# Kernel tuning notes

Hardware: AMD Instinct MI355X
Metric: run time of the kernel (lower is better)

The kernel has to match this reference:

```python
import jax, jax.numpy as jnp
import numpy as np

EPS = 1e-13


def _masked_softmax(logits, mask_last):
    # logits: [B, Q, K]; mask_last: [B, 1, K] float {0,1}
    # Faithful to torch source: multiply logits by mask (NOT additive -inf),
    # softmax, re-mask, renormalize.
    p = jax.nn.softmax(logits * mask_last, axis=-1) * mask_last
    return p / (jnp.sum(p, axis=-1, keepdims=True) + EPS)


def setup_inputs() -> dict:
    key = jax.random.key(0)
    k1, k2, k3, k4 = jax.random.split(key, 4)
    B, LA, LB, H = 16, 1024, 1024, 512
    premise_batch = jax.random.normal(k1, (B, LA, H), dtype=jnp.float32)
    hypothesis_batch = jax.random.normal(k2, (B, LB, H), dtype=jnp.float32)
    premise_mask = jax.random.randint(k3, (B, LA), 0, 2).astype(jnp.float32)
    hypothesis_mask = jax.random.randint(k4, (B, LB), 0, 2).astype(jnp.float32)
    # avoid fully-masked rows (degenerate)
    premise_mask = premise_mask.at[:, 0].set(1.0)
    hypothesis_mask = hypothesis_mask.at[:, 0].set(1.0)
    return {
        "premise_batch": premise_batch,
        "premise_mask": premise_mask,
        "hypothesis_batch": hypothesis_batch,
        "hypothesis_mask": hypothesis_mask,
    }


def reference(premise_batch, premise_mask, hypothesis_batch, hypothesis_mask):
    # sim[b,i,j] = <a_i, b_j>
    sim = jnp.einsum("bih,bjh->bij", premise_batch, hypothesis_batch)
    prem_hyp_attn = _masked_softmax(sim, hypothesis_mask[:, None, :])           # [B,LA,LB]
    hyp_prem_attn = _masked_softmax(sim.transpose(0, 2, 1), premise_mask[:, None, :])  # [B,LB,LA]
    attended_premises = jnp.einsum("bij,bjh->bih", prem_hyp_attn, hypothesis_batch)
    attended_premises = attended_premises * premise_mask[:, :, None]
    attended_hypotheses = jnp.einsum("bji,bjh->bih", hyp_prem_attn.transpose(0, 2, 1), premise_batch)
    attended_hypotheses = attended_hypotheses * hypothesis_mask[:, :, None]
    return (attended_premises, attended_hypotheses)
```

## Files before the change

### kernel.cpp

```cpp
#include <hip/hip_runtime.h>
#include <hip/hip_fp16.h>
#include <math.h>

#define NB   16
#define SLA  1024
#define SLB  1024
#define HH   512

typedef __attribute__((ext_vector_type(4))) float  f32x4;
typedef __attribute__((ext_vector_type(8))) short  s16x8;
typedef __attribute__((ext_vector_type(4))) int    i32x4;

#define QS    (6.5f / 127.f)
#define QINVS (127.f / 6.5f)

__device__ __forceinline__ unsigned short f2bf(float x){
  unsigned u = __float_as_uint(x);
  u += 0x7fffu + ((u >> 16) & 1u);
  return (unsigned short)(u >> 16);
}
__device__ __forceinline__ float bf2f(unsigned short h){
  return __uint_as_float(((unsigned)h) << 16);
}
__device__ __forceinline__ float h2f(unsigned short h){
  return __half2float(__ushort_as_half(h));
}
__device__ __forceinline__ unsigned fkey(float f){
  unsigned u = __float_as_uint(f);
  return ((int)u < 0) ? ~u : (u | 0x80000000u);
}
__device__ __forceinline__ float funkey(unsigned k){
  return __uint_as_float((k & 0x80000000u) ? (k & 0x7fffffffu) : ~k);
}

__device__ __forceinline__ void gl2lds16(const void* g, void* l){
  __builtin_amdgcn_global_load_lds(
      (__attribute__((address_space(1))) unsigned int*)(unsigned long long)(size_t)g,
      (__attribute__((address_space(3))) unsigned int*)(unsigned int)(size_t)l,
      16, 0, 0);
}

__global__ __launch_bounds__(256) void scan_kernel(
    const float* __restrict__ pmask, const float* __restrict__ hmask,
    int* __restrict__ pIdx, int* __restrict__ hIdx,
    int* __restrict__ pCnt, int* __restrict__ hCnt,
    int* __restrict__ pPad, int* __restrict__ hPad,
    unsigned* __restrict__ rowMaxU, unsigned* __restrict__ colMaxU,
    float* __restrict__ colSum)
{
  __shared__ int ps[256];
  const int b     = blockIdx.x;
  const int which = blockIdx.y;
  const int t     = threadIdx.x;
  const float* m = (which ? hmask : pmask) + b * 1024;
  int* idx = (which ? hIdx : pIdx) + b * 1024;
  int* cnt = which ? hCnt : pCnt;
  int* pad = which ? hPad : pPad;

  #pragma unroll
  for (int v = 0; v < 4; ++v){
    int g = b * 1024 + t + v * 256;
    if (which == 0){
      rowMaxU[g] = 0u;
    } else {
      colMaxU[g] = 0u;
      colSum[g]  = 0.f;
    }
  }

  int f[4], s = 0;
  #pragma unroll
  for (int e = 0; e < 4; ++e){
    f[e] = m[t * 4 + e] > 0.5f ? 1 : 0;
    s += f[e];
  }
  ps[t] = s;
  __syncthreads();
  for (int off = 1; off < 256; off <<= 1){
    int v = (t >= off) ? ps[t - off] : 0;
    __syncthreads();
    ps[t] += v;
    __syncthreads();
  }
  int pos = ps[t] - s;
  #pragma unroll
  for (int e = 0; e < 4; ++e){
    if (f[e]) idx[pos++] = t * 4 + e;
  }
  if (t == 0){
    int total = ps[255];
    cnt[b] = total;
    pad[b] = (total + 127) & ~127;
  }
}

__global__ __launch_bounds__(256) void zero_out_kernel(
    const float* __restrict__ pmask, const float* __restrict__ hmask,
    float* __restrict__ out)
{
  const int r = blockIdx.x * 4 + (threadIdx.x >> 6);
  const int side = r >> 14;
  const int b    = (r >> 10) & 15;
  const int row  = r & 1023;
  const float mv = (side ? hmask : pmask)[b * 1024 + row];
  if (mv > 0.5f) return;
  float4 z = {0.f, 0.f, 0.f, 0.f};
  float* p = out + (size_t)side * NB * SLA * HH
                 + ((size_t)b * 1024 + row) * 512 + (threadIdx.x & 63) * 8;
  *(float4*)p = z;
  *(float4*)(p + 4) = z;
}

__global__ __launch_bounds__(256) void cvt_gather_kernel(
    const float* __restrict__ prem, const float* __restrict__ hyp,
    const int* __restrict__ pIdx, const int* __restrict__ hIdx,
    const int* __restrict__ pCnt, const int* __restrict__ hCnt,
    const int* __restrict__ pPad, const int* __restrict__ hPad,
    char* __restrict__ premD1, char* __restrict__ premD0,
    char* __restrict__ hypD1,  char* __restrict__ hypD0,
    unsigned short* __restrict__ PremT, unsigned short* __restrict__ HypT)
{
  __shared__ unsigned short tv[64][72];
  __shared__ int sIdx[64];

  const int tensor = blockIdx.z >> 4;
  const int b  = blockIdx.z & 15;
  const int l0 = blockIdx.y * 64;
  const int h0 = blockIdx.x * 64;
  const int t  = threadIdx.x;

  const int cnt = tensor ? hCnt[b] : pCnt[b];
  const int pad = tensor ? hPad[b] : pPad[b];
  if (l0 >= pad) return;

  const float* X = tensor ? hyp : prem;
  const int* idx = (tensor ? hIdx : pIdx) + b * 1024;
  char* D1 = tensor ? hypD1 : premD1;
  char* D0 = tensor ? hypD0 : premD0;
  unsigned short* XT = tensor ? HypT : PremT;

  if (t < 64){
    int jc = l0 + t;
    sIdx[t] = (jc < cnt) ? idx[jc] : -1;
  }
  __syncthreads();

  #pragma unroll
  for (int it = 0; it < 4; ++it){
    int r = (t >> 4) + it * 16;
    int c = (t & 15) * 4;
    int orig = sIdx[r];
    float4 x = {0.f, 0.f, 0.f, 0.f};
    if (orig >= 0)
      x = *(const float4*)(X + ((size_t)b * 1024 + orig) * HH + h0 + c);
    float xv[4] = {x.x, x.y, x.z, x.w};
    char d1v[4], d0v[4];
    #pragma unroll
    for (int e = 0; e < 4; ++e){
      float xs = xv[e] * QINVS;
      float x1 = rintf(xs);
      x1 = fminf(127.f, fmaxf(-127.f, x1));
      float x0 = rintf((xs - x1) * 256.f);
      x0 = fminf(127.f, fmaxf(-128.f, x0));
      d1v[e] = (char)(int)x1;
      d0v[e] = (char)(int)x0;
      tv[c + e][r] = f2bf(xv[e]);
    }
    size_t go = ((size_t)b * 1024 + l0 + r) * HH + h0 + c;
    *(char4*)(D1 + go) = make_char4(d1v[0], d1v[1], d1v[2], d1v[3]);
    *(char4*)(D0 + go) = make_char4(d0v[0], d0v[1], d0v[2], d0v[3]);
  }
  __syncthreads();
  const int w   = t >> 2;
  const int seg = (t & 3) * 16;
  const uint4* src = (const uint4*)&tv[w][seg];
  uint4* dst = (uint4*)(XT + ((size_t)b * HH + h0 + w) * 1024 + l0 + seg);
  dst[0] = src[0];
  dst[1] = src[1];
}

__global__ __launch_bounds__(256, 3) void sim_gemm_v5_kernel(
    const char* __restrict__ premD1, const char* __restrict__ premD0,
    const char* __restrict__ hypD1,  const char* __restrict__ hypD0,
    const int* __restrict__ pCnt, const int* __restrict__ hCnt,
    const int* __restrict__ pPad, const int* __restrict__ hPad,
    unsigned short* __restrict__ simH,
    unsigned* __restrict__ rowMaxU, unsigned* __restrict__ colMaxU)
{
  __shared__ char sA1[128 * 64];
  __shared__ char sA0[128 * 64];
  __shared__ char sB1[64 * 64];
  __shared__ char sB0[64 * 64];

  const int b  = blockIdx.z;
  const int i0 = blockIdx.y * 128;
  const int j0 = blockIdx.x * 64;
  const int t  = threadIdx.x;

  const int pc = pCnt[b], hc = hCnt[b];
  if (i0 >= pPad[b] || j0 >= hPad[b]) return;

  const char* A1 = premD1 + ((size_t)b * 1024 + i0) * HH;
  const char* A0 = premD0 + ((size_t)b * 1024 + i0) * HH;
  const char* B1 = hypD1  + ((size_t)b * 1024 + j0) * HH;
  const char* B0 = hypD0  + ((size_t)b * 1024 + j0) * HH;

  const int sr = t >> 2;
  const int gc = ((t & 3) ^ (sr & 3)) * 16;
  const int lco = (t & 3) * 16;

  const int lane = t & 63;
  const int wr = (t >> 7) & 1;
  const int wc = (t >> 6) & 1;
  const int q  = lane >> 4;
  const int ln = lane & 15;
  const int fo = (q ^ (ln & 3)) * 16;

  i32x4 acc1[4][2], accc[4][2];
  #pragma unroll
  for (int mt = 0; mt < 4; ++mt)
    #pragma unroll
    for (int nt = 0; nt < 2; ++nt){
      acc1[mt][nt] = (i32x4){0, 0, 0, 0};
      accc[mt][nt] = (i32x4){0, 0, 0, 0};
    }

  for (int k0 = 0; k0 < HH; k0 += 64){
    __syncthreads();
    {
      const size_t goA = (size_t)sr * HH + k0 + gc;
      gl2lds16(A1 + goA, &sA1[sr * 64 + lco]);
      gl2lds16(A0 + goA, &sA0[sr * 64 + lco]);
      const size_t goA2 = (size_t)(64 + sr) * HH + k0 + gc;
      gl2lds16(A1 + goA2, &sA1[(64 + sr) * 64 + lco]);
      gl2lds16(A0 + goA2, &sA0[(64 + sr) * 64 + lco]);
      gl2lds16(B1 + goA, &sB1[sr * 64 + lco]);
      gl2lds16(B0 + goA, &sB0[sr * 64 + lco]);
    }
    __syncthreads();

    i32x4 af[4], bf1[2], bf0[2];
    #pragma unroll
    for (int mt = 0; mt < 4; ++mt)
      af[mt] = *(const i32x4*)&sA1[(wr * 64 + mt * 16 + ln) * 64 + fo];
    #pragma unroll
    for (int nt = 0; nt < 2; ++nt)
      bf1[nt] = *(const i32x4*)&sB1[(wc * 32 + nt * 16 + ln) * 64 + fo];
    #pragma unroll
    for (int mt = 0; mt < 4; ++mt)
      #pragma unroll
      for (int nt = 0; nt < 2; ++nt)
        acc1[mt][nt] = __builtin_amdgcn_mfma_i32_16x16x64_i8(af[mt], bf1[nt], acc1[mt][nt], 0, 0, 0);
    #pragma unroll
    for (int nt = 0; nt < 2; ++nt)
      bf0[nt] = *(const i32x4*)&sB0[(wc * 32 + nt * 16 + ln) * 64 + fo];
    #pragma unroll
    for (int mt = 0; mt < 4; ++mt)
      #pragma unroll
      for (int nt = 0; nt < 2; ++nt)
        accc[mt][nt] = __builtin_amdgcn_mfma_i32_16x16x64_i8(af[mt], bf0[nt], accc[mt][nt], 0, 0, 0);
    #pragma unroll
    for (int mt = 0; mt < 4; ++mt)
      af[mt] = *(const i32x4*)&sA0[(wr * 64 + mt * 16 + ln) * 64 + fo];
    #pragma unroll
    for (int mt = 0; mt < 4; ++mt)
      #pragma unroll
      for (int nt = 0; nt < 2; ++nt)
        accc[mt][nt] = __builtin_amdgcn_mfma_i32_16x16x64_i8(af[mt], bf1[nt], accc[mt][nt], 0, 0, 0);
  }

  const float S2 = QS * QS;
  unsigned short* simb = simH + ((size_t)b * SLA + i0) * SLB + j0;

  float rmx[16];
  #pragma unroll
  for (int e = 0; e < 16; ++e) rmx[e] = -1e30f;
  float cmx[2];
  cmx[0] = -1e30f; cmx[1] = -1e30f;

  #pragma unroll
  for (int mt = 0; mt < 4; ++mt){
    #pragma unroll
    for (int nt = 0; nt < 2; ++nt){
      int col = wc * 32 + nt * 16 + ln;
      bool colv = (j0 + col) < hc;
      #pragma unroll
      for (int rr = 0; rr < 4; ++rr){
        int row = wr * 64 + mt * 16 + q * 4 + rr;
        float f = S2 * ((float)acc1[mt][nt][rr] + (float)accc[mt][nt][rr] * 0.00390625f);
        simb[(size_t)row * SLB + col] = __half_as_ushort(__float2half(f));
        rmx[mt * 4 + rr] = fmaxf(rmx[mt * 4 + rr], colv ? f : -1e30f);
        cmx[nt] = fmaxf(cmx[nt], (i0 + row) < pc ? f : -1e30f);
      }
    }
  }

  #pragma unroll
  for (int e = 0; e < 16; ++e){
    float v = rmx[e];
    v = fmaxf(v, __shfl_xor(v, 1));
    v = fmaxf(v, __shfl_xor(v, 2));
    v = fmaxf(v, __shfl_xor(v, 4));
    v = fmaxf(v, __shfl_xor(v, 8));
    if (ln == 0){
      int row = wr * 64 + (e >> 2) * 16 + q * 4 + (e & 3);
      if (i0 + row < pc)
        atomicMax(rowMaxU + b * 1024 + i0 + row, fkey(v));
    }
  }
  #pragma unroll
  for (int nt = 0; nt < 2; ++nt){
    float v = cmx[nt];
    v = fmaxf(v, __shfl_xor(v, 16));
    v = fmaxf(v, __shfl_xor(v, 32));
    if (q == 0){
      int col = wc * 32 + nt * 16 + ln;
      if (j0 + col < hc)
        atomicMax(colMaxU + b * 1024 + j0 + col, fkey(v));
    }
  }
}

__global__ __launch_bounds__(256) void build_pt_kernel(
    const unsigned short* __restrict__ simH,
    const unsigned* __restrict__ colMaxU,
    const int* __restrict__ pCnt, const int* __restrict__ hCnt,
    const int* __restrict__ pPad, const int* __restrict__ hPad,
    unsigned short* __restrict__ PhypT, float* __restrict__ colSum)
{
  __shared__ unsigned short tp[64][72];
  __shared__ float sCM[64];

  const int b  = blockIdx.z;
  const int i0 = blockIdx.y * 64;
  const int j0 = blockIdx.x * 64;
  const int t  = threadIdx.x;

  const int pc = pCnt[b], hc = hCnt[b];
  if (i0 >= pPad[b] || j0 >= hPad[b]) return;

  if (t < 64) sCM[t] = funkey(colMaxU[b * 1024 + j0 + t]);
  __syncthreads();

  const unsigned short* sb = simH + (size_t)b * SLA * SLB;
  #pragma unroll
  for (int it = 0; it < 4; ++it){
    int r = (t >> 4) + it * 16;
    int c = (t & 15) * 4;
    uint2 u = *(const uint2*)(sb + (size_t)(i0 + r) * SLB + j0 + c);
    float s0 = h2f((unsigned short)(u.x & 0xffff));
    float s1 = h2f((unsigned short)(u.x >> 16));
    float s2 = h2f((unsigned short)(u.y & 0xffff));
    float s3 = h2f((unsigned short)(u.y >> 16));
    bool vi = (i0 + r) < pc;
    tp[c + 0][r] = f2bf((vi && (j0 + c + 0) < hc) ? __expf(s0 - sCM[c+0]) : 0.f);
    tp[c + 1][r] = f2bf((vi && (j0 + c + 1) < hc) ? __expf(s1 - sCM[c+1]) : 0.f);
    tp[c + 2][r] = f2bf((vi && (j0 + c + 2) < hc) ? __expf(s2 - sCM[c+2]) : 0.f);
    tp[c + 3][r] = f2bf((vi && (j0 + c + 3) < hc) ? __expf(s3 - sCM[c+3]) : 0.f);
  }
  __syncthreads();
  const int w   = t >> 2;
  const int seg = (t & 3) * 16;
  const uint4* src = (const uint4*)&tp[w][seg];
  uint4 u0 = src[0], u1 = src[1];
  uint4* dst = (uint4*)(PhypT + ((size_t)b * 1024 + j0 + w) * 1024 + i0 + seg);
  dst[0] = u0;
  dst[1] = u1;

  const unsigned short* us0 = (const unsigned short*)&u0;
  const unsigned short* us1 = (const unsigned short*)&u1;
  float cs = 0.f;
  #pragma unroll
  for (int e = 0; e < 8; ++e) cs += bf2f(us0[e]);
  #pragma unroll
  for (int e = 0; e < 8; ++e) cs += bf2f(us1[e]);
  cs += __shfl_xor(cs, 1);
  cs += __shfl_xor(cs, 2);
  if ((t & 3) == 0 && (j0 + w) < hc)
    atomicAdd(colSum + b * 1024 + j0 + w, cs);
}

__global__ __launch_bounds__(256, 4) void av2_kernel(
    const unsigned short* __restrict__ simH,
    const unsigned short* __restrict__ PhypT,
    const unsigned short* __restrict__ HypT, const unsigned short* __restrict__ PremT,
    const unsigned* __restrict__ rowMaxU, const float* __restrict__ colSum,
    const int* __restrict__ pIdx, const int* __restrict__ hIdx,
    const int* __restrict__ pCnt, const int* __restrict__ hCnt,
    const int* __restrict__ pPad, const int* __restrict__ hPad,
    float* __restrict__ out)
{
  __shared__ unsigned short sA[128 * 64];
  __shared__ unsigned short sB[128 * 64];
  __shared__ float sRM[128];
  __shared__ float sScale[128];
  __shared__ int   sIdx[128];

  const int side = blockIdx.z >> 4;
  const int b    = blockIdx.z & 15;
  const int m0   = blockIdx.y * 128;
  const int n0   = blockIdx.x * 128;
  const int t    = threadIdx.x;

  const int cnt  = side ? hCnt[b] : pCnt[b];
  const int hc   = hCnt[b];
  const int mpad = side ? hPad[b] : pPad[b];
  const int kpad = side ? pPad[b] : hPad[b];
  if (m0 >= mpad) return;

  const int* idx = (side ? hIdx : pIdx) + b * 1024;
  float* o = out + (size_t)side * NB * SLA * HH + (size_t)b * 1024 * 512;

  if (t < 128){
    sIdx[t] = idx[m0 + t];
    if (side){
      sScale[t] = 1.f / colSum[b * 1024 + m0 + t];
    } else {
      sRM[t] = funkey(rowMaxU[b * 1024 + m0 + t]);
    }
  }

  const int wv = t >> 6;
  const int L  = t & 63;
  const int lr = L >> 3;
  const int sw = L & 7;
  const int gkc = (sw ^ lr) * 8;

  const int ar  = t >> 1;
  const int akh = (t & 1) * 32;

  const int lane = t & 63;
  const int wr = (t >> 7) & 1;
  const int wc = (t >> 6) & 1;
  const int q  = lane >> 4;
  const int ln = lane & 15;
  const int fsw = ln & 7;

  const unsigned short* simb  = simH  + (size_t)b * 1024 * 1024;
  const unsigned short* Ahyp  = PhypT + (size_t)b * 1024 * 1024;
  const unsigned short* Bt    = (side ? PremT : HypT) + (size_t)b * 512 * 1024;

  float rs = 0.f;

  f32x4 acc[4][4];
  #pragma unroll
  for (int mt = 0; mt < 4; ++mt)
    #pragma unroll
    for (int nt = 0; nt < 4; ++nt)
      acc[mt][nt] = (f32x4){0.f, 0.f, 0.f, 0.f};

  for (int k0 = 0; k0 < kpad; k0 += 64){
    __syncthreads();
    if (side == 0){
      #pragma unroll
      for (int s = 0; s < 4; ++s){
        int row = wv * 32 + s * 8 + lr;
        gl2lds16(Bt + (size_t)(n0 + row) * 1024 + k0 + gkc, &sB[row * 64 + sw * 8]);
      }
      const unsigned short* sp = simb + (size_t)(m0 + ar) * 1024 + k0 + akh;
      float rm = sRM[ar];
      #pragma unroll
      for (int cc = 0; cc < 4; ++cc){
        uint4 u = *(const uint4*)(sp + cc * 8);
        unsigned uw[4] = {u.x, u.y, u.z, u.w};
        int kb = k0 + akh + cc * 8;
        unsigned short pb[8];
        #pragma unroll
        for (int d = 0; d < 4; ++d){
          float v0 = h2f((unsigned short)(uw[d] & 0xffff));
          float v1 = h2f((unsigned short)(uw[d] >> 16));
          float p0 = (kb + d * 2 + 0) < hc ? __expf(v0 - rm) : 0.f;
          float p1 = (kb + d * 2 + 1) < hc ? __expf(v1 - rm) : 0.f;
          rs += p0 + p1;
          pb[d * 2]     = f2bf(p0);
          pb[d * 2 + 1] = f2bf(p1);
        }
        uint4 w;
        w.x = (unsigned)pb[0] | ((unsigned)pb[1] << 16);
        w.y = (unsigned)pb[2] | ((unsigned)pb[3] << 16);
        w.z = (unsigned)pb[4] | ((unsigned)pb[5] << 16);
        w.w = (unsigned)pb[6] | ((unsigned)pb[7] << 16);
        int c   = (t & 1) * 4 + cc;
        int pos = c ^ (ar & 7);
        *(uint4*)&sA[ar * 64 + pos * 8] = w;
      }
    } else {
      #pragma unroll
      for (int s = 0; s < 4; ++s){
        int row = wv * 32 + s * 8 + lr;
        gl2lds16(Ahyp + (size_t)(m0 + row) * 1024 + k0 + gkc, &sA[row * 64 + sw * 8]);
        gl2lds16(Bt   + (size_t)(n0 + row) * 1024 + k0 + gkc, &sB[row * 64 + sw * 8]);
      }
    }
    __syncthreads();

    #pragma unroll
    for (int h = 0; h < 2; ++h){
      s16x8 af[4], bfr[4];
      #pragma unroll
      for (int mt = 0; mt < 4; ++mt){
        int r = wr * 64 + mt * 16 + ln;
        af[mt] = *(const s16x8*)&sA[r * 64 + (((h << 2) + q) ^ fsw) * 8];
      }
      #pragma unroll
      for (int nt = 0; nt < 4; ++nt){
        int r = wc * 64 + nt * 16 + ln;
        bfr[nt] = *(const s16x8*)&sB[r * 64 + (((h << 2) + q) ^ fsw) * 8];
      }
      #pragma unroll
      for (int mt = 0; mt < 4; ++mt)
        #pragma unroll
        for (int nt = 0; nt < 4; ++nt)
          acc[mt][nt] = __builtin_amdgcn_mfma_f32_16x16x32_bf16(af[mt], bfr[nt], acc[mt][nt], 0, 0, 0);
    }
  }

  if (side == 0){
    rs += __shfl_xor(rs, 1);
    __syncthreads();
    if ((t & 1) == 0) sScale[ar] = 1.f / rs;
    __syncthreads();
  }

  #pragma unroll
  for (int mt = 0; mt < 4; ++mt)
    #pragma unroll
    for (int nt = 0; nt < 4; ++nt){
      int col = n0 + wc * 64 + nt * 16 + ln;
      #pragma unroll
      for (int rr = 0; rr < 4; ++rr){
        int rowL = wr * 64 + mt * 16 + q * 4 + rr;
        if (m0 + rowL < cnt)
          o[(size_t)sIdx[rowL] * 512 + col] = acc[mt][nt][rr] * sScale[rowL];
      }
    }
}

extern "C" void kernel_launch(void* const* d_in, const int* in_sizes, int n_in,
                              void* d_out, int out_size, void* d_ws, size_t ws_size,
                              hipStream_t stream)
{
  const float* prem  = (const float*)d_in[0];
  const float* pmask = (const float*)d_in[1];
  const float* hyp   = (const float*)d_in[2];
  const float* hmask = (const float*)d_in[3];
  float* out = (float*)d_out;

  char* ws = (char*)d_ws;
  unsigned short* simH = (unsigned short*)(ws);
  unsigned* rowMaxU = (unsigned*)(ws + 67108864);
  unsigned* colMaxU = (unsigned*)(ws + 67108864 + 2 * 65536);
  float*    colSum  = (float*)(ws + 67108864 + 3 * 65536);
  int* pIdx = (int*)(ws + 67108864 + 4 * 65536);
  int* hIdx = (int*)(ws + 67108864 + 5 * 65536);
  int* pCnt = (int*)(ws + 67108864 + 6 * 65536);
  int* hCnt = (int*)(ws + 67108864 + 6 * 65536 + 256);
  int* pPad = (int*)(ws + 67108864 + 6 * 65536 + 512);
  int* hPad = (int*)(ws + 67108864 + 6 * 65536 + 768);
  const size_t base2 = 67108864 + 4 * 65536 + 1048576;
  char* premD1 = (char*)(ws + base2);
  char* premD0 = (char*)(ws + base2 + 8388608);
  char* hypD1  = (char*)(ws + base2 + 16777216);
  char* hypD0  = (char*)(ws + base2 + 25165824);
  unsigned short* PremT = (unsigned short*)(ws + base2 + 33554432);
  unsigned short* HypT  = (unsigned short*)(ws + base2 + 50331648);
  unsigned short* PhypT = (unsigned short*)(ws + base2);
  const size_t need = base2 + 100663296;
  if (ws_size < need) return;

  scan_kernel<<<dim3(16, 2), 256, 0, stream>>>(pmask, hmask, pIdx, hIdx,
                                               pCnt, hCnt, pPad, hPad,
                                               rowMaxU, colMaxU, colSum);
  zero_out_kernel<<<dim3(8192), 256, 0, stream>>>(pmask, hmask, out);
  cvt_gather_kernel<<<dim3(8, 16, 32), 256, 0, stream>>>(
      prem, hyp, pIdx, hIdx, pCnt, hCnt, pPad, hPad,
      premD1, premD0, hypD1, hypD0, PremT, HypT);
  sim_gemm_v5_kernel<<<dim3(16, 8, NB), 256, 0, stream>>>(
      premD1, premD0, hypD1, hypD0, pCnt, hCnt, pPad, hPad,
      simH, rowMaxU, colMaxU);
  build_pt_kernel<<<dim3(16, 16, NB), 256, 0, stream>>>(
      simH, colMaxU, pCnt, hCnt, pPad, hPad, PhypT, colSum);
  av2_kernel<<<dim3(4, 8, 32), 256, 0, stream>>>(
      simH, PhypT, HypT, PremT, rowMaxU, colSum,
      pIdx, hIdx, pCnt, hCnt, pPad, hPad, out);
}
```

Baseline: 210.1 us.

## Write transposed sim in GEMM epilogue and drop separate build_pt pass

The sim GEMM epilogue now also writes a transposed fp16 copy of the similarity tile through an LDS staging buffer that reuses the operand shared memory. The later attention-value kernel treats both sides the same way, computing exp and row sums on the fly from either simH or simT. This removes the build_pt kernel and its colSum atomics, trading that extra full pass over the sim matrix for additional stores in the GEMM and exp work on the hypothesis side of the AV kernel.

```diff
diff --git a/kernel.cpp b/kernel.cpp
--- a/kernel.cpp
+++ b/kernel.cpp
@@ -45,8 +45,7 @@
     int* __restrict__ pIdx, int* __restrict__ hIdx,
     int* __restrict__ pCnt, int* __restrict__ hCnt,
     int* __restrict__ pPad, int* __restrict__ hPad,
-    unsigned* __restrict__ rowMaxU, unsigned* __restrict__ colMaxU,
-    float* __restrict__ colSum)
+    unsigned* __restrict__ rowMaxU, unsigned* __restrict__ colMaxU)
 {
   __shared__ int ps[256];
   const int b     = blockIdx.x;
@@ -64,7 +63,6 @@
       rowMaxU[g] = 0u;
     } else {
       colMaxU[g] = 0u;
-      colSum[g]  = 0.f;
     }
   }
 
@@ -179,18 +177,28 @@
   dst[1] = src[1];
 }
 
-__global__ __launch_bounds__(256, 3) void sim_gemm_v5_kernel(
+__global__ __launch_bounds__(256, 3) void sim_gemm_v6_kernel(
     const char* __restrict__ premD1, const char* __restrict__ premD0,
     const char* __restrict__ hypD1,  const char* __restrict__ hypD0,
     const int* __restrict__ pCnt, const int* __restrict__ hCnt,
     const int* __restrict__ pPad, const int* __restrict__ hPad,
-    unsigned short* __restrict__ simH,
+    unsigned short* __restrict__ simH, unsigned short* __restrict__ simT,
     unsigned* __restrict__ rowMaxU, unsigned* __restrict__ colMaxU)
 {
-  __shared__ char sA1[128 * 64];
-  __shared__ char sA0[128 * 64];
-  __shared__ char sB1[64 * 64];
-  __shared__ char sB0[64 * 64];
+  union __align__(16) Smem {
+    struct {
+      char A1[128 * 64];
+      char A0[128 * 64];
+      char B1[64 * 64];
+      char B0[64 * 64];
+    } g;
+    unsigned short tp[64][136];
+  };
+  __shared__ Smem su;
+#define sA1 (su.g.A1)
+#define sA0 (su.g.A0)
+#define sB1 (su.g.B1)
+#define sB0 (su.g.B0)
 
   const int b  = blockIdx.z;
   const int i0 = blockIdx.y * 128;
@@ -278,21 +286,41 @@
   float cmx[2];
   cmx[0] = -1e30f; cmx[1] = -1e30f;
 
+  __syncthreads();
+
   #pragma unroll
   for (int mt = 0; mt < 4; ++mt){
     #pragma unroll
     for (int nt = 0; nt < 2; ++nt){
       int col = wc * 32 + nt * 16 + ln;
       bool colv = (j0 + col) < hc;
+      unsigned short hv[4];
       #pragma unroll
       for (int rr = 0; rr < 4; ++rr){
         int row = wr * 64 + mt * 16 + q * 4 + rr;
         float f = S2 * ((float)acc1[mt][nt][rr] + (float)accc[mt][nt][rr] * 0.00390625f);
-        simb[(size_t)row * SLB + col] = __half_as_ushort(__float2half(f));
+        unsigned short hb = __half_as_ushort(__float2half(f));
+        simb[(size_t)row * SLB + col] = hb;
+        hv[rr] = hb;
         rmx[mt * 4 + rr] = fmaxf(rmx[mt * 4 + rr], colv ? f : -1e30f);
         cmx[nt] = fmaxf(cmx[nt], (i0 + row) < pc ? f : -1e30f);
       }
-    }
+      uint2 w;
+      w.x = (unsigned)hv[0] | ((unsigned)hv[1] << 16);
+      w.y = (unsigned)hv[2] | ((unsigned)hv[3] << 16);
+      *(uint2*)&su.tp[col][wr * 64 + mt * 16 + q * 4] = w;
+    }
+  }
+  __syncthreads();
+  {
+    const int jr  = t >> 2;
+    const int seg = (t & 3) * 32;
+    const uint4* src = (const uint4*)&su.tp[jr][seg];
+    uint4* dst = (uint4*)(simT + ((size_t)b * SLB + j0 + jr) * SLA + i0 + seg);
+    dst[0] = src[0];
+    dst[1] = src[1];
+    dst[2] = src[2];
+    dst[3] = src[3];
   }
 
   #pragma unroll
@@ -319,72 +347,17 @@
         atomicMax(colMaxU + b * 1024 + j0 + col, fkey(v));
     }
   }
-}
-
-__global__ __launch_bounds__(256) void build_pt_kernel(
+#undef sA1
+#undef sA0
+#undef sB1
+#undef sB0
+}
+
+__global__ __launch_bounds__(256, 4) void av3_kernel(
     const unsigned short* __restrict__ simH,
-    const unsigned* __restrict__ colMaxU,
-    const int* __restrict__ pCnt, const int* __restrict__ hCnt,
-    const int* __restrict__ pPad, const int* __restrict__ hPad,
-    unsigned short* __restrict__ PhypT, float* __restrict__ colSum)
-{
-  __shared__ unsigned short tp[64][72];
-  __shared__ float sCM[64];
-
-  const int b  = blockIdx.z;
-  const int i0 = blockIdx.y * 64;
-  const int j0 = blockIdx.x * 64;
-  const int t  = threadIdx.x;
-
-  const int pc = pCnt[b], hc = hCnt[b];
-  if (i0 >= pPad[b] || j0 >= hPad[b]) return;
-
-  if (t < 64) sCM[t] = funkey(colMaxU[b * 1024 + j0 + t]);
-  __syncthreads();
-
-  const unsigned short* sb = simH + (size_t)b * SLA * SLB;
-  #pragma unroll
-  for (int it = 0; it < 4; ++it){
-    int r = (t >> 4) + it * 16;
-    int c = (t & 15) * 4;
-    uint2 u = *(const uint2*)(sb + (size_t)(i0 + r) * SLB + j0 + c);
-    float s0 = h2f((unsigned short)(u.x & 0xffff));
-    float s1 = h2f((unsigned short)(u.x >> 16));
-    float s2 = h2f((unsigned short)(u.y & 0xffff));
-    float s3 = h2f((unsigned short)(u.y >> 16));
-    bool vi = (i0 + r) < pc;
-    tp[c + 0][r] = f2bf((vi && (j0 + c + 0) < hc) ? __expf(s0 - sCM[c+0]) : 0.f);
-    tp[c + 1][r] = f2bf((vi && (j0 + c + 1) < hc) ? __expf(s1 - sCM[c+1]) : 0.f);
-    tp[c + 2][r] = f2bf((vi && (j0 + c + 2) < hc) ? __expf(s2 - sCM[c+2]) : 0.f);
-    tp[c + 3][r] = f2bf((vi && (j0 + c + 3) < hc) ? __expf(s3 - sCM[c+3]) : 0.f);
-  }
-  __syncthreads();
-  const int w   = t >> 2;
-  const int seg = (t & 3) * 16;
-  const uint4* src = (const uint4*)&tp[w][seg];
-  uint4 u0 = src[0], u1 = src[1];
-  uint4* dst = (uint4*)(PhypT + ((size_t)b * 1024 + j0 + w) * 1024 + i0 + seg);
-  dst[0] = u0;
-  dst[1] = u1;
-
-  const unsigned short* us0 = (const unsigned short*)&u0;
-  const unsigned short* us1 = (const unsigned short*)&u1;
-  float cs = 0.f;
-  #pragma unroll
-  for (int e = 0; e < 8; ++e) cs += bf2f(us0[e]);
-  #pragma unroll
-  for (int e = 0; e < 8; ++e) cs += bf2f(us1[e]);
-  cs += __shfl_xor(cs, 1);
-  cs += __shfl_xor(cs, 2);
-  if ((t & 3) == 0 && (j0 + w) < hc)
-    atomicAdd(colSum + b * 1024 + j0 + w, cs);
-}
-
-__global__ __launch_bounds__(256, 4) void av2_kernel(
-    const unsigned short* __restrict__ simH,
-    const unsigned short* __restrict__ PhypT,
+    const unsigned short* __restrict__ simT,
     const unsigned short* __restrict__ HypT, const unsigned short* __restrict__ PremT,
-    const unsigned* __restrict__ rowMaxU, const float* __restrict__ colSum,
+    const unsigned* __restrict__ rowMaxU, const unsigned* __restrict__ colMaxU,
     const int* __restrict__ pIdx, const int* __restrict__ hIdx,
     const int* __restrict__ pCnt, const int* __restrict__ hCnt,
     const int* __restrict__ pPad, const int* __restrict__ hPad,
@@ -403,9 +376,9 @@
   const int t    = threadIdx.x;
 
   const int cnt  = side ? hCnt[b] : pCnt[b];
-  const int hc   = hCnt[b];
   const int mpad = side ? hPad[b] : pPad[b];
   const int kpad = side ? pPad[b] : hPad[b];
+  const int kcnt = side ? pCnt[b] : hCnt[b];
   if (m0 >= mpad) return;
 
   const int* idx = (side ? hIdx : pIdx) + b * 1024;
@@ -413,11 +386,7 @@
 
   if (t < 128){
     sIdx[t] = idx[m0 + t];
-    if (side){
-      sScale[t] = 1.f / colSum[b * 1024 + m0 + t];
-    } else {
-      sRM[t] = funkey(rowMaxU[b * 1024 + m0 + t]);
-    }
+    sRM[t]  = funkey((side ? colMaxU : rowMaxU)[b * 1024 + m0 + t]);
   }
 
   const int wv = t >> 6;
@@ -436,9 +405,8 @@
   const int ln = lane & 15;
   const int fsw = ln & 7;
 
-  const unsigned short* simb  = simH  + (size_t)b * 1024 * 1024;
-  const unsigned short* Ahyp  = PhypT + (size_t)b * 1024 * 1024;
-  const unsigned short* Bt    = (side ? PremT : HypT) + (size_t)b * 512 * 1024;
+  const unsigned short* As = (side ? simT : simH) + (size_t)b * 1024 * 1024;
+  const unsigned short* Bt = (side ? PremT : HypT) + (size_t)b * 512 * 1024;
 
   float rs = 0.f;
 
@@ -451,13 +419,13 @@
 
   for (int k0 = 0; k0 < kpad; k0 += 64){
     __syncthreads();
-    if (side == 0){
-      #pragma unroll
-      for (int s = 0; s < 4; ++s){
-        int row = wv * 32 + s * 8 + lr;
-        gl2lds16(Bt + (size_t)(n0 + row) * 1024 + k0 + gkc, &sB[row * 64 + sw * 8]);
-      }
-      const unsigned short* sp = simb + (size_t)(m0 + ar) * 1024 + k0 + akh;
+    #pragma unroll
+    for (int s = 0; s < 4; ++s){
+      int row = wv * 32 + s * 8 + lr;
+      gl2lds16(Bt + (size_t)(n0 + row) * 1024 + k0 + gkc, &sB[row * 64 + sw * 8]);
+    }
+    {
+      const unsigned short* sp = As + (size_t)(m0 + ar) * 1024 + k0 + akh;
       float rm = sRM[ar];
       #pragma unroll
       for (int cc = 0; cc < 4; ++cc){
@@ -469,8 +437,8 @@
         for (int d = 0; d < 4; ++d){
           float v0 = h2f((unsigned short)(uw[d] & 0xffff));
           float v1 = h2f((unsigned short)(uw[d] >> 16));
-          float p0 = (kb + d * 2 + 0) < hc ? __expf(v0 - rm) : 0.f;
-          float p1 = (kb + d * 2 + 1) < hc ? __expf(v1 - rm) : 0.f;
+          float p0 = (kb + d * 2 + 0) < kcnt ? __expf(v0 - rm) : 0.f;
+          float p1 = (kb + d * 2 + 1) < kcnt ? __expf(v1 - rm) : 0.f;
           rs += p0 + p1;
           pb[d * 2]     = f2bf(p0);
           pb[d * 2 + 1] = f2bf(p1);
@@ -484,13 +452,6 @@
         int pos = c ^ (ar & 7);
         *(uint4*)&sA[ar * 64 + pos * 8] = w;
       }
-    } else {
-      #pragma unroll
-      for (int s = 0; s < 4; ++s){
-        int row = wv * 32 + s * 8 + lr;
-        gl2lds16(Ahyp + (size_t)(m0 + row) * 1024 + k0 + gkc, &sA[row * 64 + sw * 8]);
-        gl2lds16(Bt   + (size_t)(n0 + row) * 1024 + k0 + gkc, &sB[row * 64 + sw * 8]);
-      }
     }
     __syncthreads();
 
@@ -515,12 +476,10 @@
     }
   }
 
-  if (side == 0){
-    rs += __shfl_xor(rs, 1);
-    __syncthreads();
-    if ((t & 1) == 0) sScale[ar] = 1.f / rs;
-    __syncthreads();
-  }
+  rs += __shfl_xor(rs, 1);
+  __syncthreads();
+  if ((t & 1) == 0) sScale[ar] = 1.f / rs;
+  __syncthreads();
 
   #pragma unroll
   for (int mt = 0; mt < 4; ++mt)
@@ -548,9 +507,9 @@
 
   char* ws = (char*)d_ws;
   unsigned short* simH = (unsigned short*)(ws);
+  unsigned short* simT = (unsigned short*)(ws + 33554432);
   unsigned* rowMaxU = (unsigned*)(ws + 67108864);
   unsigned* colMaxU = (unsigned*)(ws + 67108864 + 2 * 65536);
-  float*    colSum  = (float*)(ws + 67108864 + 3 * 65536);
   int* pIdx = (int*)(ws + 67108864 + 4 * 65536);
   int* hIdx = (int*)(ws + 67108864 + 5 * 65536);
   int* pCnt = (int*)(ws + 67108864 + 6 * 65536);
@@ -564,23 +523,20 @@
   char* hypD0  = (char*)(ws + base2 + 25165824);
   unsigned short* PremT = (unsigned short*)(ws + base2 + 33554432);
   unsigned short* HypT  = (unsigned short*)(ws + base2 + 50331648);
-  unsigned short* PhypT = (unsigned short*)(ws + base2);
   const size_t need = base2 + 100663296;
   if (ws_size < need) return;
 
   scan_kernel<<<dim3(16, 2), 256, 0, stream>>>(pmask, hmask, pIdx, hIdx,
                                                pCnt, hCnt, pPad, hPad,
-                                               rowMaxU, colMaxU, colSum);
+                                               rowMaxU, colMaxU);
   zero_out_kernel<<<dim3(8192), 256, 0, stream>>>(pmask, hmask, out);
   cvt_gather_kernel<<<dim3(8, 16, 32), 256, 0, stream>>>(
       prem, hyp, pIdx, hIdx, pCnt, hCnt, pPad, hPad,
       premD1, premD0, hypD1, hypD0, PremT, HypT);
-  sim_gemm_v5_kernel<<<dim3(16, 8, NB), 256, 0, stream>>>(
+  sim_gemm_v6_kernel<<<dim3(16, 8, NB), 256, 0, stream>>>(
       premD1, premD0, hypD1, hypD0, pCnt, hCnt, pPad, hPad,
-      simH, rowMaxU, colMaxU);
-  build_pt_kernel<<<dim3(16, 16, NB), 256, 0, stream>>>(
-      simH, colMaxU, pCnt, hCnt, pPad, hPad, PhypT, colSum);
-  av2_kernel<<<dim3(4, 8, 32), 256, 0, stream>>>(
-      simH, PhypT, HypT, PremT, rowMaxU, colSum,
+      simH, simT, rowMaxU, colMaxU);
+  av3_kernel<<<dim3(4, 8, 32), 256, 0, stream>>>(
+      simH, simT, HypT, PremT, rowMaxU, colMaxU,
       pIdx, hIdx, pCnt, hCnt, pPad, hPad, out);
 }
```

After: 211.0 us. No clear change (+0.4%).
